# Performance work log

Measured on AMD Instinct MI355X. Metric: run time of the kernel, lower is better.

Reference implementation:

```python
import jax, jax.numpy as jnp
import numpy as np
from jax import lax

DK = 3            # deformable kernel size
K = DK * DK       # sampling points per pixel per group
PAD = DK // 2


def conv2d(x, w, b, pad):
    y = lax.conv_general_dilated(x, w, (1, 1), [(pad, pad), (pad, pad)],
                                 dimension_numbers=('NCHW', 'OIHW', 'NCHW'))
    return y + b[None, :, None, None]


def setup_inputs() -> dict:
    key = jax.random.key(0)
    ks = jax.random.split(key, 7)
    B, C, H, W = 2, 64, 128, 128
    nf, out_nc = 64, 64
    s_in = 1.0 / np.sqrt(C * 9)
    s_om = 0.05 / np.sqrt(nf * 9)   # small offsets/masks, as after training-ish init
    s_dc = 1.0 / np.sqrt(C * K)
    return {
        'x':    jax.random.normal(ks[0], (B, C, H, W), jnp.float32),
        'w_in': jax.random.normal(ks[1], (nf, C, 3, 3), jnp.float32) * s_in,
        'b_in': jnp.zeros((nf,), jnp.float32),
        'w_om': jax.random.normal(ks[2], (C * 3 * K, nf, 3, 3), jnp.float32) * s_om,
        'b_om': jnp.zeros((C * 3 * K,), jnp.float32),
        'w_dc': jax.random.normal(ks[3], (out_nc, C, DK, DK), jnp.float32) * s_dc,
        'b_dc': jnp.zeros((out_nc,), jnp.float32),
    }


def _deform_conv(feat, off, msk, w_dc, b_dc):
    # feat: [B,C,H,W]; off: [B,C,K,2,H,W] (y,x per kernel pt); msk: [B,C,K,H,W]
    B, C, H, W = feat.shape
    # base sampling grid: kernel taps relative to output pixel (padding = PAD)
    ky = (jnp.arange(K) // DK - PAD).astype(jnp.float32)   # [K]
    kx = (jnp.arange(K) % DK - PAD).astype(jnp.float32)
    hh = jnp.arange(H, dtype=jnp.float32)
    ww = jnp.arange(W, dtype=jnp.float32)
    py = off[:, :, :, 0] + ky[None, None, :, None, None] + hh[None, None, None, :, None]
    px = off[:, :, :, 1] + kx[None, None, :, None, None] + ww[None, None, None, None, :]

    y0f = jnp.floor(py); x0f = jnp.floor(px)
    wy1 = py - y0f; wx1 = px - x0f
    y0 = y0f.astype(jnp.int32); x0 = x0f.astype(jnp.int32)
    feat_flat = feat.reshape(B, C, H * W)

    def gather(yi, xi):
        valid = (yi >= 0) & (yi < H) & (xi >= 0) & (xi < W)
        idx = jnp.clip(yi, 0, H - 1) * W + jnp.clip(xi, 0, W - 1)  # [B,C,K,H,W]
        v = jnp.take_along_axis(feat_flat, idx.reshape(B, C, -1), axis=2)
        return v.reshape(B, C, K, H, W) * valid.astype(feat.dtype)

    sampled = ((1 - wy1) * (1 - wx1) * gather(y0, x0)
               + (1 - wy1) * wx1 * gather(y0, x0 + 1)
               + wy1 * (1 - wx1) * gather(y0 + 1, x0)
               + wy1 * wx1 * gather(y0 + 1, x0 + 1))
    mod = sampled * msk                                   # [B,C,K,H,W]
    O = w_dc.shape[0]
    out = jnp.einsum('bckhw,ock->bohw', mod, w_dc.reshape(O, C, K))
    return out + b_dc[None, :, None, None]


def reference(x, w_in, b_in, w_om, b_om, w_dc, b_dc):
    B, _, H, W = x.shape
    C = w_dc.shape[1]
    feat = jax.nn.leaky_relu(conv2d(x, w_in, b_in, 1), 0.1)   # in_conv
    om = conv2d(feat, w_om, b_om, 1)                          # offset_mask
    off = om[:, :C * 2 * K].reshape(B, C, K, 2, H, W)
    msk = jax.nn.sigmoid(om[:, C * 2 * K:]).reshape(B, C, K, H, W)
    return jax.nn.relu(_deform_conv(feat, off, msk, w_dc, b_dc))
```

## Files before the change

### kernel.cpp

```cpp
#include <hip/hip_runtime.h>

typedef unsigned short u16;
typedef __bf16 bf16x8 __attribute__((ext_vector_type(8)));
typedef float f32x4 __attribute__((ext_vector_type(4)));

__device__ __forceinline__ float b2f(u16 u) {
    unsigned int x = ((unsigned int)u) << 16;
    float f; __builtin_memcpy(&f, &x, 4); return f;
}
__device__ __forceinline__ u16 f2b(float f) {
    unsigned int x; __builtin_memcpy(&x, &f, 4);
    unsigned int r = (x + 0x7fffu + ((x >> 16) & 1u)) >> 16;
    return (u16)r;
}

__global__ void k_prep(const float* __restrict__ w_om, const float* __restrict__ b_om,
                       const float* __restrict__ w_in, const float* __restrict__ w_dc,
                       const float* __restrict__ b_dc,
                       u16* __restrict__ wv_om3, float* __restrict__ bv_om,
                       u16* __restrict__ wv_in2, u16* __restrict__ wv_dc2,
                       float* __restrict__ bv_dc)
{
    int blk = blockIdx.x, t = threadIdx.x;
    if (blk < 2048) {
        int m = blk, c = m >> 5, q = m & 31, g = m >> 7, ml = m & 127;
        bool pad = q >= 27;
        int src = 0;
        if (!pad) { int j = q / 9, k = q - j * 9; src = (j < 2) ? ((c * 9 + k) * 2 + j) : (1152 + c * 9 + k); }
        for (int idx = t; idx < 576; idx += 128) {
            int tap = idx >> 6, ci = idx & 63;
            int run = ci >> 3, j = ci & 7;
            u16 v = pad ? (u16)0 : f2b(w_om[(size_t)src * 576 + ci * 9 + tap]);
            wv_om3[(((size_t)g * 9 + tap) * 8 + run) * 1024 + ml * 8 + j] = v;
        }
        if (t == 0) bv_om[m] = pad ? 0.f : b_om[src];
    } else if (blk < 2112) {
        int m = blk - 2048;
        for (int idx = t; idx < 576; idx += 128) {
            int tap = idx >> 6, ci = idx & 63;
            int run = ci >> 3, j = ci & 7;
            wv_in2[(((size_t)tap * 8 + run) * 64 + m) * 8 + j] = f2b(w_in[(size_t)m * 576 + ci * 9 + tap]);
        }
    } else {
        int m = blk - 2112;
        for (int idx = t; idx < 576; idx += 128)
            wv_dc2[((size_t)(idx >> 3) * 64 + m) * 8 + (idx & 7)] = f2b(w_dc[(size_t)m * 576 + idx]);
        if (t == 0) bv_dc[m] = b_dc[m];
    }
}

__global__ void k_transpose(const float* __restrict__ x, u16* __restrict__ x_t)
{
    __shared__ u16 sm[64 * 136];
    int row = blockIdx.x;
    int b = row >> 7, y = row & 127;
    int t = threadIdx.x;
    for (int it = 0; it < 4; ++it) {
        int chunk = it * 256 + t;
        int ci = chunk >> 4, part = chunk & 15;
        const float4* src = (const float4*)(x + (((size_t)(b * 64 + ci) * 128 + y) * 128) + part * 8);
        float4 v0 = src[0], v1 = src[1];
        u16 tmp[8] = { f2b(v0.x), f2b(v0.y), f2b(v0.z), f2b(v0.w),
                       f2b(v1.x), f2b(v1.y), f2b(v1.z), f2b(v1.w) };
        *(uint4*)(&sm[ci * 136 + part * 8]) = *(uint4*)tmp;
    }
    __syncthreads();
    int xx = t >> 1, half = t & 1;
    u16 tmp[32];
#pragma unroll
    for (int cc = 0; cc < 32; ++cc) tmp[cc] = sm[(half * 32 + cc) * 136 + xx];
    u16* dst = x_t + (((size_t)(b * 130) + y + 1) * 130 + (xx + 1)) * 64 + half * 32;
#pragma unroll
    for (int j = 0; j < 4; ++j) ((uint4*)dst)[j] = ((uint4*)tmp)[j];
}

__global__ __launch_bounds__(256) void k_conv1(
    const u16* __restrict__ wv_in2, const float* __restrict__ b_in,
    const u16* __restrict__ x_t, u16* __restrict__ feat_t, u16* __restrict__ feat_c)
{
    __shared__ char smem[51072];
    float* om = (float*)smem;
    int row = blockIdx.x, b = row >> 7, y = row & 127;
    int t = threadIdx.x, lane = t & 63, wv = t >> 6;
    int wm = wv >> 1, wn = wv & 1, lm = lane & 15, kg = lane >> 4;
    f32x4 acc[2][4] = {};
    const u16* fb = x_t + (size_t)b * 130 * 130 * 64;
    for (int id = t; id < 3120; id += 256) {
        int r3 = id / 1040, rem = id - r3 * 1040;
        int pix = rem >> 3, r2 = rem & 7;
        uint4 v = *(const uint4*)(fb + ((size_t)(y + r3) * 130) * 64 + rem * 8);
        *(uint4*)(smem + (((r2 * 3 + r3) * 133 + pix) << 4)) = v;
    }
    const u16* ab = wv_in2;
    int arow = (wm * 32 + lm) * 8;
    bf16x8 af[3][2];
#pragma unroll
    for (int mt = 0; mt < 2; ++mt)
        af[0][mt] = *(const bf16x8*)(ab + (size_t)kg * 512 + arow + mt * 128);
#pragma unroll
    for (int mt = 0; mt < 2; ++mt)
        af[1][mt] = *(const bf16x8*)(ab + (size_t)(4 + kg) * 512 + arow + mt * 128);
    __syncthreads();
#pragma unroll
    for (int s = 0; s < 18; ++s) {
        if (s < 16) {
            int s2 = s + 2, tap2 = s2 >> 1, run2 = (s2 & 1) * 4 + kg;
#pragma unroll
            for (int mt = 0; mt < 2; ++mt)
                af[(s + 2) % 3][mt] = *(const bf16x8*)(ab + ((size_t)tap2 * 8 + run2) * 512 + arow + mt * 128);
        }
        int tap = s >> 1, run = (s & 1) * 4 + kg;
        int dy = tap / 3, dx = tap - dy * 3;
        bf16x8 bf[4];
#pragma unroll
        for (int nt = 0; nt < 4; ++nt)
            bf[nt] = *(const bf16x8*)(smem + (((run * 3 + dy) * 133 + wn * 64 + nt * 16 + lm + dx) << 4));
#pragma unroll
        for (int mt = 0; mt < 2; ++mt)
#pragma unroll
            for (int nt = 0; nt < 4; ++nt)
                acc[mt][nt] = __builtin_amdgcn_mfma_f32_16x16x32_bf16(af[s % 3][mt], bf[nt], acc[mt][nt], 0, 0, 0);
    }
    __syncthreads();
#pragma unroll
    for (int mt = 0; mt < 2; ++mt)
#pragma unroll
        for (int nt = 0; nt < 4; ++nt)
#pragma unroll
            for (int i = 0; i < 4; ++i) {
                int m = wm * 32 + mt * 16 + kg * 4 + i;
                int n = wn * 64 + nt * 16 + lm;
                float v = acc[mt][nt][i] + b_in[m];
                v = v > 0.f ? v : 0.1f * v;
                om[m * 132 + n] = v;
            }
    __syncthreads();
    for (int it = 0; it < 32; ++it) {
        int item = it * 256 + t, ci = item >> 7, xx = item & 127;
        feat_c[(((size_t)(ci * 2 + b)) * 128 + y) * 128 + xx] = f2b(om[ci * 132 + xx]);
    }
    {
        int xx = t >> 1, half = t & 1;
        u16 tmp[32];
#pragma unroll
        for (int cc = 0; cc < 32; ++cc) tmp[cc] = f2b(om[(half * 32 + cc) * 132 + xx]);
        u16* dst = feat_t + (((size_t)(b * 130) + y + 1) * 130 + (xx + 1)) * 64 + half * 32;
#pragma unroll
        for (int j = 0; j < 4; ++j) ((uint4*)dst)[j] = ((uint4*)tmp)[j];
    }
}

__global__ __launch_bounds__(256) void k_conv2(
    const u16* __restrict__ wv_om3, const float* __restrict__ bv_om,
    const u16* __restrict__ feat_t, const u16* __restrict__ feat_c,
    u16* __restrict__ mod_t)
{
    __shared__ char smem[51072];
    u16* omb = (u16*)smem;
    u16* modl = (u16*)(smem + 28512);
    u16* ft   = (u16*)(smem + 38240);
    int g = blockIdx.x, row = blockIdx.y;
    int b = row >> 7, y = row & 127;
    int t = threadIdx.x, lane = t & 63, wv = t >> 6;
    int wm = wv >> 1, wn = wv & 1, lm = lane & 15, kg = lane >> 4;
    f32x4 acc[4][4] = {};
    const u16* fb = feat_t + (size_t)b * 130 * 130 * 64;
    for (int id = t; id < 3120; id += 256) {
        int r3 = id / 1040, rem = id - r3 * 1040;
        int pix = rem >> 3, r2 = rem & 7;
        uint4 v = *(const uint4*)(fb + ((size_t)(y + r3) * 130) * 64 + rem * 8);
        *(uint4*)(smem + (((r2 * 3 + r3) * 133 + pix) << 4)) = v;
    }
    const u16* ab = wv_om3 + (size_t)g * 9 * 8192;
    int arow = (wm * 64 + lm) * 8;
    bf16x8 af[3][4];
#pragma unroll
    for (int mt = 0; mt < 4; ++mt)
        af[0][mt] = *(const bf16x8*)(ab + (size_t)kg * 1024 + arow + mt * 128);
#pragma unroll
    for (int mt = 0; mt < 4; ++mt)
        af[1][mt] = *(const bf16x8*)(ab + (size_t)(4 + kg) * 1024 + arow + mt * 128);
    __syncthreads();
#pragma unroll
    for (int s = 0; s < 18; ++s) {
        if (s < 16) {
            int s2 = s + 2, tap2 = s2 >> 1, run2 = (s2 & 1) * 4 + kg;
#pragma unroll
            for (int mt = 0; mt < 4; ++mt)
                af[(s + 2) % 3][mt] = *(const bf16x8*)(ab + ((size_t)tap2 * 8 + run2) * 1024 + arow + mt * 128);
        }
        int tap = s >> 1, run = (s & 1) * 4 + kg;
        int dy = tap / 3, dx = tap - dy * 3;
        bf16x8 bf[4];
#pragma unroll
        for (int nt = 0; nt < 4; ++nt)
            bf[nt] = *(const bf16x8*)(smem + (((run * 3 + dy) * 133 + wn * 64 + nt * 16 + lm + dx) << 4));
#pragma unroll
        for (int mt = 0; mt < 4; ++mt)
#pragma unroll
            for (int nt = 0; nt < 4; ++nt)
                acc[mt][nt] = __builtin_amdgcn_mfma_f32_16x16x32_bf16(af[s % 3][mt], bf[nt], acc[mt][nt], 0, 0, 0);
    }
    __syncthreads();
#pragma unroll
    for (int mt = 0; mt < 4; ++mt)
#pragma unroll
        for (int nt = 0; nt < 4; ++nt)
#pragma unroll
            for (int i = 0; i < 4; ++i) {
                int m = wm * 64 + mt * 16 + kg * 4 + i;
                int q = m & 31, cl = m >> 5;
                if (q < 27) {
                    int n = wn * 64 + nt * 16 + lm;
                    omb[(cl * 27 + q) * 132 + n] = f2b(acc[mt][nt][i] + bv_om[g * 128 + m]);
                }
            }
    if (t < 40) {
        int rr = t >> 1, side = t & 1;
        uint4 z = {0, 0, 0, 0};
        *(uint4*)(ft + rr * 144 + side * 136) = z;
    }
    for (int ch = t; ch < 320; ch += 256) {
        int cl = ch / 80, rem = ch - cl * 80;
        int r = rem >> 4, part = rem & 15;
        int gy = y + r - 2;
        uint4 v = {0, 0, 0, 0};
        if ((unsigned)gy < 128u)
            v = *(const uint4*)(feat_c + ((size_t)((g * 4 + cl) * 2 + b)) * 16384 + gy * 128 + part * 8);
        *(uint4*)(ft + (cl * 5 + r) * 144 + 8 + part * 8) = v;
    }
    __syncthreads();
    for (int it = 0; it < 18; ++it) {
        int item = it * 256 + t;
        int ckl = item >> 7, xx = item & 127;
        int cl = ckl / 9, k = ckl - cl * 9;
        float offy = b2f(omb[(cl * 27 + k) * 132 + xx]);
        float offx = b2f(omb[(cl * 27 + 9 + k) * 132 + xx]);
        float mv   = b2f(omb[(cl * 27 + 18 + k) * 132 + xx]);
        float msk = 1.f / (1.f + __expf(-mv));
        float fy = floorf(offy), fx = floorf(offx);
        float wy = offy - fy, wx = offx - fx;
        int r0 = k / 3 + 1 + (int)fy;
        int c0 = 7 + xx + (k - (k / 3) * 3) + (int)fx;
        const u16* base = ft + (cl * 5 + r0) * 144 + c0;
        float v00 = b2f(base[0]),   v01 = b2f(base[1]);
        float v10 = b2f(base[144]), v11 = b2f(base[145]);
        float h0 = v00 + wx * (v01 - v00);
        float h1 = v10 + wx * (v11 - v10);
        float s = h0 + wy * (h1 - h0);
        modl[xx * 38 + ckl] = f2b(s * msk);
    }
    __syncthreads();
    {
        unsigned int* mo = (unsigned int*)mod_t;
        const unsigned int* ml = (const unsigned int*)modl;
        for (int w = t; w < 2304; w += 256) {
            int pix = w / 18, widx = w - pix * 18;
            mo[((size_t)(row * 128 + pix)) * 288 + g * 18 + widx] = ml[pix * 19 + widx];
        }
    }
}

__global__ __launch_bounds__(256) void k_gemm3(
    const u16* __restrict__ wv_dc2, const float* __restrict__ bv_dc,
    const u16* __restrict__ mod_t, float* __restrict__ out)
{
    __shared__ char smem[32768];
    int row = blockIdx.x, b = row >> 7, y = row & 127;
    int t = threadIdx.x, lane = t & 63, wv = t >> 6;
    int wm = wv >> 1, wn = wv & 1, lm = lane & 15, kg = lane >> 4;
    f32x4 acc[2][4] = {};
    size_t p0 = (size_t)row * 128;
    int pixs[4], runs[4], slots[4];
#pragma unroll
    for (int ii = 0; ii < 4; ++ii) {
        int ch = ii * 256 + t;
        pixs[ii] = ch >> 3; runs[ii] = ch & 7;
        slots[ii] = (runs[ii] << 7) + (pixs[ii] ^ runs[ii]);
    }
#pragma unroll
    for (int ii = 0; ii < 4; ++ii)
        *(uint4*)(smem + slots[ii] * 16) =
            *(const uint4*)(mod_t + (p0 + pixs[ii]) * 576 + runs[ii] * 8);
    __syncthreads();
#pragma unroll
    for (int kc = 0; kc < 9; ++kc) {
        char* bb = smem + (kc & 1) * 16384;
        uint4 pre[4];
        if (kc < 8) {
#pragma unroll
            for (int ii = 0; ii < 4; ++ii)
                pre[ii] = *(const uint4*)(mod_t + (p0 + pixs[ii]) * 576 + (kc + 1) * 64 + runs[ii] * 8);
        }
#pragma unroll
        for (int ks = 0; ks < 2; ++ks) {
            int run = ks * 4 + kg;
            bf16x8 af[2], bf[4];
#pragma unroll
            for (int mt = 0; mt < 2; ++mt)
                af[mt] = *(const bf16x8*)(wv_dc2 + (((size_t)kc * 8 + run) * 64 + wm * 32 + mt * 16 + lm) * 8);
#pragma unroll
            for (int nt = 0; nt < 4; ++nt) {
                int n = wn * 64 + nt * 16 + lm;
                bf[nt] = *(const bf16x8*)(bb + ((run << 7) + (n ^ run)) * 16);
            }
#pragma unroll
            for (int mt = 0; mt < 2; ++mt)
#pragma unroll
                for (int nt = 0; nt < 4; ++nt)
                    acc[mt][nt] = __builtin_amdgcn_mfma_f32_16x16x32_bf16(af[mt], bf[nt], acc[mt][nt], 0, 0, 0);
        }
        if (kc < 8) {
            char* nb = smem + ((kc & 1) ^ 1) * 16384;
#pragma unroll
            for (int ii = 0; ii < 4; ++ii)
                *(uint4*)(nb + slots[ii] * 16) = pre[ii];
        }
        __syncthreads();
    }
#pragma unroll
    for (int mt = 0; mt < 2; ++mt)
#pragma unroll
        for (int nt = 0; nt < 4; ++nt)
#pragma unroll
            for (int i = 0; i < 4; ++i) {
                int o = wm * 32 + mt * 16 + kg * 4 + i;
                int n = wn * 64 + nt * 16 + lm;
                float v = acc[mt][nt][i] + bv_dc[o];
                v = v > 0.f ? v : 0.f;
                out[(((size_t)(b * 64 + o)) * 128 + y) * 128 + n] = v;
            }
}

extern "C" void kernel_launch(void* const* d_in, const int* in_sizes, int n_in,
                              void* d_out, int out_size, void* d_ws, size_t ws_size,
                              hipStream_t stream)
{
    (void)in_sizes; (void)n_in; (void)out_size; (void)ws_size;
    const float* x    = (const float*)d_in[0];
    const float* w_in = (const float*)d_in[1];
    const float* b_in = (const float*)d_in[2];
    const float* w_om = (const float*)d_in[3];
    const float* b_om = (const float*)d_in[4];
    const float* w_dc = (const float*)d_in[5];
    const float* b_dc = (const float*)d_in[6];
    char* ws = (char*)d_ws;
    u16*   x_t    = (u16*)(ws);
    u16*   feat_t = (u16*)(ws + 4326400);
    u16*   feat_c = (u16*)(ws + 8652800);
    u16*   wv_om3 = (u16*)(ws + 12847104);
    u16*   wv_in2 = (u16*)(ws + 15206400);
    u16*   wv_dc2 = (u16*)(ws + 15280128);
    float* bv_om  = (float*)(ws + 15353856);
    float* bv_dc  = (float*)(ws + 15362048);
    u16*   mod_t  = (u16*)(ws + 15362304);

    hipMemsetAsync(ws, 0, 8652800, stream);
    hipLaunchKernelGGL(k_prep, dim3(2176), dim3(128), 0, stream,
                       w_om, b_om, w_in, w_dc, b_dc, wv_om3, bv_om, wv_in2, wv_dc2, bv_dc);
    hipLaunchKernelGGL(k_transpose, dim3(256), dim3(256), 0, stream, x, x_t);
    hipLaunchKernelGGL(k_conv1, dim3(256), dim3(256), 0, stream,
                       wv_in2, b_in, x_t, feat_t, feat_c);
    hipLaunchKernelGGL(k_conv2, dim3(16, 256), dim3(256), 0, stream,
                       wv_om3, bv_om, feat_t, feat_c, mod_t);
    hipLaunchKernelGGL(k_gemm3, dim3(256), dim3(256), 0, stream,
                       wv_dc2, bv_dc, mod_t, (float*)d_out);
}
```

Measured before the change: 221.2 us.

## Shrink conv2 LDS footprint via row-staged B tiles and split gemm3 across pixel halves

In k_conv2, the B operand is now staged two input rows at a time. The third row is loaded into registers during the second phase and then overwrites row 0, which cuts LDS from about 51KB to about 36KB. The offset/mask buffer is re-laid out pixel-major with packed 32-bit stores, and the mod buffer now aliases the offset buffer, which adds an extra barrier and keeps the results in registers. k_gemm3 is split into two blocks per row (64 pixels each) with halved LDS, to raise occupancy and grid parallelism. The tradeoffs are extra synchronisations and register pressure from the staged row data.

Result: faster. 214.3 us (-3.1%).

```diff
diff --git a/kernel.cpp b/kernel.cpp
--- a/kernel.cpp
+++ b/kernel.cpp
@@ -155,21 +155,21 @@
     const u16* __restrict__ feat_t, const u16* __restrict__ feat_c,
     u16* __restrict__ mod_t)
 {
-    __shared__ char smem[51072];
-    u16* omb = (u16*)smem;
-    u16* modl = (u16*)(smem + 28512);
-    u16* ft   = (u16*)(smem + 38240);
+    __shared__ char smem[35968];
+    u16* omb  = (u16*)smem;
+    u16* modl = (u16*)smem;
+    u16* ft   = (u16*)(smem + 30208);
     int g = blockIdx.x, row = blockIdx.y;
     int b = row >> 7, y = row & 127;
     int t = threadIdx.x, lane = t & 63, wv = t >> 6;
     int wm = wv >> 1, wn = wv & 1, lm = lane & 15, kg = lane >> 4;
     f32x4 acc[4][4] = {};
     const u16* fb = feat_t + (size_t)b * 130 * 130 * 64;
-    for (int id = t; id < 3120; id += 256) {
-        int r3 = id / 1040, rem = id - r3 * 1040;
+    for (int id = t; id < 2080; id += 256) {
+        int ds = id / 1040, rem = id - ds * 1040;
         int pix = rem >> 3, r2 = rem & 7;
-        uint4 v = *(const uint4*)(fb + ((size_t)(y + r3) * 130) * 64 + rem * 8);
-        *(uint4*)(smem + (((r2 * 3 + r3) * 133 + pix) << 4)) = v;
+        uint4 v = *(const uint4*)(fb + ((size_t)(y + ds) * 130) * 64 + rem * 8);
+        *(uint4*)(smem + (((ds * 8 + r2) * 133 + pix) << 4)) = v;
     }
     const u16* ab = wv_om3 + (size_t)g * 9 * 8192;
     int arow = (wm * 64 + lm) * 8;
@@ -182,19 +182,68 @@
         af[1][mt] = *(const bf16x8*)(ab + (size_t)(4 + kg) * 1024 + arow + mt * 128);
     __syncthreads();
 #pragma unroll
-    for (int s = 0; s < 18; ++s) {
+    for (int s = 0; s < 6; ++s) {
+        int s2 = s + 2, tap2 = s2 >> 1, run2 = (s2 & 1) * 4 + kg;
+#pragma unroll
+        for (int mt = 0; mt < 4; ++mt)
+            af[s2 % 3][mt] = *(const bf16x8*)(ab + ((size_t)tap2 * 8 + run2) * 1024 + arow + mt * 128);
+        int tap = s >> 1, run = (s & 1) * 4 + kg, dx = tap;
+        bf16x8 bf[4];
+#pragma unroll
+        for (int nt = 0; nt < 4; ++nt)
+            bf[nt] = *(const bf16x8*)(smem + ((run * 133 + wn * 64 + nt * 16 + lm + dx) << 4));
+#pragma unroll
+        for (int mt = 0; mt < 4; ++mt)
+#pragma unroll
+            for (int nt = 0; nt < 4; ++nt)
+                acc[mt][nt] = __builtin_amdgcn_mfma_f32_16x16x32_bf16(af[s % 3][mt], bf[nt], acc[mt][nt], 0, 0, 0);
+    }
+    __syncthreads();
+    uint4 r2v[5];
+#pragma unroll
+    for (int j = 0; j < 5; ++j) {
+        int id = j * 256 + t;
+        if (id < 1040) r2v[j] = *(const uint4*)(fb + ((size_t)(y + 2) * 130) * 64 + id * 8);
+    }
+#pragma unroll
+    for (int s = 6; s < 12; ++s) {
+        int s2 = s + 2, tap2 = s2 >> 1, run2 = (s2 & 1) * 4 + kg;
+#pragma unroll
+        for (int mt = 0; mt < 4; ++mt)
+            af[s2 % 3][mt] = *(const bf16x8*)(ab + ((size_t)tap2 * 8 + run2) * 1024 + arow + mt * 128);
+        int tap = s >> 1, run = (s & 1) * 4 + kg, dx = tap - 3;
+        bf16x8 bf[4];
+#pragma unroll
+        for (int nt = 0; nt < 4; ++nt)
+            bf[nt] = *(const bf16x8*)(smem + (((8 + run) * 133 + wn * 64 + nt * 16 + lm + dx) << 4));
+#pragma unroll
+        for (int mt = 0; mt < 4; ++mt)
+#pragma unroll
+            for (int nt = 0; nt < 4; ++nt)
+                acc[mt][nt] = __builtin_amdgcn_mfma_f32_16x16x32_bf16(af[s % 3][mt], bf[nt], acc[mt][nt], 0, 0, 0);
+    }
+#pragma unroll
+    for (int j = 0; j < 5; ++j) {
+        int id = j * 256 + t;
+        if (id < 1040) {
+            int pix = id >> 3, r2 = id & 7;
+            *(uint4*)(smem + ((r2 * 133 + pix) << 4)) = r2v[j];
+        }
+    }
+    __syncthreads();
+#pragma unroll
+    for (int s = 12; s < 18; ++s) {
         if (s < 16) {
             int s2 = s + 2, tap2 = s2 >> 1, run2 = (s2 & 1) * 4 + kg;
 #pragma unroll
             for (int mt = 0; mt < 4; ++mt)
-                af[(s + 2) % 3][mt] = *(const bf16x8*)(ab + ((size_t)tap2 * 8 + run2) * 1024 + arow + mt * 128);
-        }
-        int tap = s >> 1, run = (s & 1) * 4 + kg;
-        int dy = tap / 3, dx = tap - dy * 3;
+                af[s2 % 3][mt] = *(const bf16x8*)(ab + ((size_t)tap2 * 8 + run2) * 1024 + arow + mt * 128);
+        }
+        int tap = s >> 1, run = (s & 1) * 4 + kg, dx = tap - 6;
         bf16x8 bf[4];
 #pragma unroll
         for (int nt = 0; nt < 4; ++nt)
-            bf[nt] = *(const bf16x8*)(smem + (((run * 3 + dy) * 133 + wn * 64 + nt * 16 + lm + dx) << 4));
+            bf[nt] = *(const bf16x8*)(smem + ((run * 133 + wn * 64 + nt * 16 + lm + dx) << 4));
 #pragma unroll
         for (int mt = 0; mt < 4; ++mt)
 #pragma unroll
@@ -203,18 +252,23 @@
     }
     __syncthreads();
 #pragma unroll
-    for (int mt = 0; mt < 4; ++mt)
-#pragma unroll
-        for (int nt = 0; nt < 4; ++nt)
-#pragma unroll
-            for (int i = 0; i < 4; ++i) {
-                int m = wm * 64 + mt * 16 + kg * 4 + i;
-                int q = m & 31, cl = m >> 5;
-                if (q < 27) {
-                    int n = wn * 64 + nt * 16 + lm;
-                    omb[(cl * 27 + q) * 132 + n] = f2b(acc[mt][nt][i] + bv_om[g * 128 + m]);
-                }
+    for (int mt = 0; mt < 4; ++mt) {
+        int cl = wm * 2 + (mt >> 1);
+        int q0 = (mt & 1) * 16 + kg * 4;
+        if (q0 != 28) {
+            float4 bs = *(const float4*)(bv_om + g * 128 + wm * 64 + mt * 16 + kg * 4);
+#pragma unroll
+            for (int nt = 0; nt < 4; ++nt) {
+                int n = wn * 64 + nt * 16 + lm;
+                unsigned int lo = (unsigned int)f2b(acc[mt][nt][0] + bs.x)
+                                | ((unsigned int)f2b(acc[mt][nt][1] + bs.y) << 16);
+                unsigned int hi = (unsigned int)f2b(acc[mt][nt][2] + bs.z)
+                                | ((unsigned int)f2b(acc[mt][nt][3] + bs.w) << 16);
+                unsigned int* p = (unsigned int*)(omb + n * 118 + cl * 28 + q0);
+                p[0] = lo; p[1] = hi;
             }
+        }
+    }
     if (t < 40) {
         int rr = t >> 1, side = t & 1;
         uint4 z = {0, 0, 0, 0};
@@ -230,13 +284,16 @@
         *(uint4*)(ft + (cl * 5 + r) * 144 + 8 + part * 8) = v;
     }
     __syncthreads();
+    u16 sres[18];
+#pragma unroll
     for (int it = 0; it < 18; ++it) {
-        int item = it * 256 + t;
-        int ckl = item >> 7, xx = item & 127;
+        int ckl = it * 2 + (t >> 7);
+        int xx = t & 127;
         int cl = ckl / 9, k = ckl - cl * 9;
-        float offy = b2f(omb[(cl * 27 + k) * 132 + xx]);
-        float offx = b2f(omb[(cl * 27 + 9 + k) * 132 + xx]);
-        float mv   = b2f(omb[(cl * 27 + 18 + k) * 132 + xx]);
+        const u16* ob = omb + xx * 118 + cl * 28;
+        float offy = b2f(ob[k]);
+        float offx = b2f(ob[9 + k]);
+        float mv   = b2f(ob[18 + k]);
         float msk = 1.f / (1.f + __expf(-mv));
         float fy = floorf(offy), fx = floorf(offx);
         float wy = offy - fy, wx = offx - fx;
@@ -248,7 +305,14 @@
         float h0 = v00 + wx * (v01 - v00);
         float h1 = v10 + wx * (v11 - v10);
         float s = h0 + wy * (h1 - h0);
-        modl[xx * 38 + ckl] = f2b(s * msk);
+        sres[it] = f2b(s * msk);
+    }
+    __syncthreads();
+#pragma unroll
+    for (int it = 0; it < 18; ++it) {
+        int ckl = it * 2 + (t >> 7);
+        int xx = t & 127;
+        modl[xx * 38 + ckl] = sres[it];
     }
     __syncthreads();
     {
@@ -265,55 +329,55 @@
     const u16* __restrict__ wv_dc2, const float* __restrict__ bv_dc,
     const u16* __restrict__ mod_t, float* __restrict__ out)
 {
-    __shared__ char smem[32768];
-    int row = blockIdx.x, b = row >> 7, y = row & 127;
+    __shared__ char smem[16384];
+    int xh = blockIdx.x, row = blockIdx.y, b = row >> 7, y = row & 127;
     int t = threadIdx.x, lane = t & 63, wv = t >> 6;
     int wm = wv >> 1, wn = wv & 1, lm = lane & 15, kg = lane >> 4;
-    f32x4 acc[2][4] = {};
-    size_t p0 = (size_t)row * 128;
-    int pixs[4], runs[4], slots[4];
-#pragma unroll
-    for (int ii = 0; ii < 4; ++ii) {
+    f32x4 acc[2][2] = {};
+    size_t p0 = (size_t)row * 128 + xh * 64;
+    int pixs[2], runs[2], slots[2];
+#pragma unroll
+    for (int ii = 0; ii < 2; ++ii) {
         int ch = ii * 256 + t;
         pixs[ii] = ch >> 3; runs[ii] = ch & 7;
-        slots[ii] = (runs[ii] << 7) + (pixs[ii] ^ runs[ii]);
-    }
-#pragma unroll
-    for (int ii = 0; ii < 4; ++ii)
+        slots[ii] = (runs[ii] << 6) + (pixs[ii] ^ runs[ii]);
+    }
+#pragma unroll
+    for (int ii = 0; ii < 2; ++ii)
         *(uint4*)(smem + slots[ii] * 16) =
             *(const uint4*)(mod_t + (p0 + pixs[ii]) * 576 + runs[ii] * 8);
     __syncthreads();
 #pragma unroll
     for (int kc = 0; kc < 9; ++kc) {
-        char* bb = smem + (kc & 1) * 16384;
-        uint4 pre[4];
+        char* bb = smem + (kc & 1) * 8192;
+        uint4 pre[2];
         if (kc < 8) {
 #pragma unroll
-            for (int ii = 0; ii < 4; ++ii)
+            for (int ii = 0; ii < 2; ++ii)
                 pre[ii] = *(const uint4*)(mod_t + (p0 + pixs[ii]) * 576 + (kc + 1) * 64 + runs[ii] * 8);
         }
 #pragma unroll
         for (int ks = 0; ks < 2; ++ks) {
             int run = ks * 4 + kg;
-            bf16x8 af[2], bf[4];
+            bf16x8 af[2], bf[2];
 #pragma unroll
             for (int mt = 0; mt < 2; ++mt)
                 af[mt] = *(const bf16x8*)(wv_dc2 + (((size_t)kc * 8 + run) * 64 + wm * 32 + mt * 16 + lm) * 8);
 #pragma unroll
-            for (int nt = 0; nt < 4; ++nt) {
-                int n = wn * 64 + nt * 16 + lm;
-                bf[nt] = *(const bf16x8*)(bb + ((run << 7) + (n ^ run)) * 16);
+            for (int nt = 0; nt < 2; ++nt) {
+                int n = wn * 32 + nt * 16 + lm;
+                bf[nt] = *(const bf16x8*)(bb + ((run << 6) + (n ^ run)) * 16);
             }
 #pragma unroll
             for (int mt = 0; mt < 2; ++mt)
 #pragma unroll
-                for (int nt = 0; nt < 4; ++nt)
+                for (int nt = 0; nt < 2; ++nt)
                     acc[mt][nt] = __builtin_amdgcn_mfma_f32_16x16x32_bf16(af[mt], bf[nt], acc[mt][nt], 0, 0, 0);
         }
         if (kc < 8) {
-            char* nb = smem + ((kc & 1) ^ 1) * 16384;
-#pragma unroll
-            for (int ii = 0; ii < 4; ++ii)
+            char* nb = smem + ((kc & 1) ^ 1) * 8192;
+#pragma unroll
+            for (int ii = 0; ii < 2; ++ii)
                 *(uint4*)(nb + slots[ii] * 16) = pre[ii];
         }
         __syncthreads();
@@ -321,14 +385,14 @@
 #pragma unroll
     for (int mt = 0; mt < 2; ++mt)
 #pragma unroll
-        for (int nt = 0; nt < 4; ++nt)
+        for (int nt = 0; nt < 2; ++nt)
 #pragma unroll
             for (int i = 0; i < 4; ++i) {
                 int o = wm * 32 + mt * 16 + kg * 4 + i;
-                int n = wn * 64 + nt * 16 + lm;
+                int n = wn * 32 + nt * 16 + lm;
                 float v = acc[mt][nt][i] + bv_dc[o];
                 v = v > 0.f ? v : 0.f;
-                out[(((size_t)(b * 64 + o)) * 128 + y) * 128 + n] = v;
+                out[(((size_t)(b * 64 + o)) * 128 + y) * 128 + xh * 64 + n] = v;
             }
 }
 
@@ -363,6 +427,6 @@
                        wv_in2, b_in, x_t, feat_t, feat_c);
     hipLaunchKernelGGL(k_conv2, dim3(16, 256), dim3(256), 0, stream,
                        wv_om3, bv_om, feat_t, feat_c, mod_t);
-    hipLaunchKernelGGL(k_gemm3, dim3(256), dim3(256), 0, stream,
+    hipLaunchKernelGGL(k_gemm3, dim3(2, 256), dim3(256), 0, stream,
                        wv_dc2, bv_dc, mod_t, (float*)d_out);
 }
```
